# Performance work log

Hardware: AMD Instinct MI355X
Metric: run time of the kernel (lower is better)

## Reference

```python
import jax, jax.numpy as jnp
import numpy as np

B, S, H, DK = 2, 2048, 16, 64
D = H * DK  # d_model = 1024


def setup_inputs() -> dict:
    key = jax.random.key(0)
    ks = jax.random.split(key, 12)
    inp = {
        "queries": jax.random.normal(ks[0], (B, S, D), jnp.float32),
        "keys": jax.random.normal(ks[1], (B, S, D), jnp.float32),
        "values": jax.random.normal(ks[2], (B, S, D), jnp.float32),
        # additive 0/1 mask (1 = masked out), causal upper-triangular
        "mask": jnp.triu(jnp.ones((S, S), jnp.float32), k=1)[None, None, :, :],
        "W_q": jax.random.normal(ks[3], (D, D), jnp.float32) / np.sqrt(D),
        "b_q": jnp.zeros((D,), jnp.float32),
        "W_k": jax.random.normal(ks[4], (D, D), jnp.float32) / np.sqrt(D),
        "b_k": jnp.zeros((D,), jnp.float32),
        "W_v": jax.random.normal(ks[5], (D, D), jnp.float32) / np.sqrt(D),
        "b_v": jnp.zeros((D,), jnp.float32),
        "W_o": jax.random.normal(ks[6], (D, D), jnp.float32) / np.sqrt(D),
        "b_o": jnp.zeros((D,), jnp.float32),
    }
    return inp


def _split_heads(x):
    # (B, S, D) -> (B, H, S, DK)
    return x.reshape(x.shape[0], x.shape[1], H, DK).transpose(0, 2, 1, 3)


def reference(queries, keys, values, mask, W_q, b_q, W_k, b_k, W_v, b_v, W_o, b_o):
    q = _split_heads(queries @ W_q + b_q)  # (B, H, S, DK)
    k = _split_heads(keys @ W_k + b_k)
    v = _split_heads(values @ W_v + b_v)
    scale = 1.0 / jnp.sqrt(jnp.asarray(DK, q.dtype))
    scores = jnp.einsum("bhqd,bhkd->bhqk", q, k) * scale  # (B, H, S, S)
    scores = scores + (-1e9) * mask
    weights = jax.nn.softmax(scores, axis=-1)
    o = jnp.einsum("bhqk,bhkd->bhqd", weights, v)  # (B, H, S, DK)
    o = o.transpose(0, 2, 1, 3).reshape(queries.shape[0], queries.shape[1], D)
    return o @ W_o + b_o
```

## Files before the change

### kernel.cpp

```cpp
#include <hip/hip_runtime.h>
#include <hip/hip_bf16.h>
#include <stdint.h>

typedef unsigned short u16;
typedef __attribute__((ext_vector_type(4))) float f32x4;
typedef __attribute__((ext_vector_type(8))) short bf16x8;

#define B_ 2
#define S_ 2048
#define H_ 16
#define D_ 1024
#define XELEMS (B_*S_*D_)
#define WELEMS (D_*D_)

__device__ __forceinline__ u16 f2bf(float f) {
  union { float f; unsigned u; } v; v.f = f;
  unsigned r = v.u + 0x7fffu + ((v.u >> 16) & 1u);
  return (u16)(r >> 16);
}

__device__ __forceinline__ void async16(const void* g, void* l) {
  __builtin_amdgcn_global_load_lds(
      (const __attribute__((address_space(1))) unsigned int*)g,
      (__attribute__((address_space(3))) unsigned int*)l, 16, 0, 0);
}

#if __has_builtin(__builtin_amdgcn_exp2f)
#define EXP2(x) __builtin_amdgcn_exp2f(x)
#else
#define EXP2(x) exp2f(x)
#endif

__device__ __forceinline__ unsigned cvtpk(float a, float b) {
  unsigned r;
  asm("v_cvt_pk_bf16_f32 %0, %1, %2" : "=v"(r) : "v"(a), "v"(b));
  return r;
}

__global__ __launch_bounds__(256) void prep_k(
    const float* __restrict__ q, const float* __restrict__ k,
    const float* __restrict__ v,
    const float* __restrict__ Wq, const float* __restrict__ Wk,
    const float* __restrict__ Wv, const float* __restrict__ Wo,
    u16* __restrict__ X, u16* __restrict__ WT) {
  const int bid = blockIdx.x;
  if (bid < 4096) {
    __shared__ float tile[32][33];
    const int z = bid >> 10, rem = bid & 1023;
    const float* W = (z == 0) ? Wq : (z == 1) ? Wk : (z == 2) ? Wv : Wo;
    u16* o = WT + z * WELEMS;
    const int r0 = (rem >> 5) << 5, c0 = (rem & 31) << 5;
    const int tx = threadIdx.x & 31, ty = threadIdx.x >> 5;
    #pragma unroll
    for (int rr = ty; rr < 32; rr += 8)
      tile[rr][tx] = W[(r0 + rr) * D_ + c0 + tx];
    __syncthreads();
    #pragma unroll
    for (int rr = ty; rr < 32; rr += 8)
      o[(c0 + rr) * D_ + r0 + tx] = f2bf(tile[tx][rr]);
  } else {
    const int cb = bid - 4096;
    const int ngrp = XELEMS / 8;
    const int total = 3 * ngrp;
    for (int i = cb * 256 + threadIdx.x; i < total; i += 1024 * 256) {
      int which = i / ngrp;
      int off = (i - which * ngrp) * 8;
      const float* src = (which == 0) ? q : (which == 1) ? k : v;
      float4 a = *(const float4*)(src + off);
      float4 b = *(const float4*)(src + off + 4);
      u16 rr[8] = {f2bf(a.x), f2bf(a.y), f2bf(a.z), f2bf(a.w),
                   f2bf(b.x), f2bf(b.y), f2bf(b.z), f2bf(b.w)};
      uint4 pk;
      pk.x = (unsigned)rr[0] | ((unsigned)rr[1] << 16);
      pk.y = (unsigned)rr[2] | ((unsigned)rr[3] << 16);
      pk.z = (unsigned)rr[4] | ((unsigned)rr[5] << 16);
      pk.w = (unsigned)rr[6] | ((unsigned)rr[7] << 16);
      *(uint4*)(X + which * XELEMS + off) = pk;
    }
  }
}

template <int MODE, int DBUF>
__device__ __forceinline__ void gemm_body(const u16* __restrict__ A,
                                          const u16* __restrict__ BT,
                                          const float* __restrict__ bias,
                                          void* __restrict__ outp,
                                          int bm, int bn) {
  constexpr int SMEM_BYTES = DBUF ? 65536 : (MODE == 2 ? 34816 : 32768);
  __shared__ __align__(16) char smem[SMEM_BYTES];
  const int tid = threadIdx.x;
  const int w = tid >> 6, l = tid & 63;
  const int wr = w >> 1, wc = w & 1;
  const int g = l >> 4, r = l & 15;
  (void)w; (void)l;

  f32x4 acc[4][4];
  #pragma unroll
  for (int i = 0; i < 4; i++)
    #pragma unroll
    for (int j = 0; j < 4; j++) acc[i][j] = (f32x4){0.f, 0.f, 0.f, 0.f};

  int dst[4], aoff[4], boff[4];
  #pragma unroll
  for (int i = 0; i < 4; i++) {
    const int o = i * 4096 + tid * 16;
    dst[i] = o;
    const int row = o >> 7;
    const int cbyte = (o & 127) ^ ((row & 7) << 4);
    aoff[i] = (bm + row) * 1024 + (cbyte >> 1);
    boff[i] = (bn + row) * 1024 + (cbyte >> 1);
  }

  if (DBUF == 0) {
    char* Ab = smem;
    char* Bb = smem + 16384;
    for (int t = 0; t < 16; ++t) {
      const int k0 = t * 64;
      #pragma unroll
      for (int i = 0; i < 4; i++) async16(A + aoff[i] + k0, Ab + dst[i]);
      #pragma unroll
      for (int i = 0; i < 4; i++) async16(BT + boff[i] + k0, Bb + dst[i]);
      __syncthreads();
      bf16x8 af[2][4], bf[2][4];
      #pragma unroll
      for (int kk = 0; kk < 2; kk++)
        #pragma unroll
        for (int mi = 0; mi < 4; mi++) {
          const int rA = wr * 64 + mi * 16 + r;
          af[kk][mi] = *(const bf16x8*)(Ab +
              ((rA * 128 + kk * 64 + g * 16) ^ ((rA & 7) << 4)));
        }
      #pragma unroll
      for (int kk = 0; kk < 2; kk++)
        #pragma unroll
        for (int ni = 0; ni < 4; ni++) {
          const int rB = wc * 64 + ni * 16 + r;
          bf[kk][ni] = *(const bf16x8*)(Bb +
              ((rB * 128 + kk * 64 + g * 16) ^ ((rB & 7) << 4)));
        }
      #pragma unroll
      for (int kk = 0; kk < 2; kk++)
        #pragma unroll
        for (int mi = 0; mi < 4; mi++)
          #pragma unroll
          for (int ni = 0; ni < 4; ni++)
            acc[mi][ni] = __builtin_amdgcn_mfma_f32_16x16x32_bf16(
                af[kk][mi], bf[kk][ni], acc[mi][ni], 0, 0, 0);
      __syncthreads();
    }
  } else {
    #pragma unroll
    for (int i = 0; i < 4; i++) {
      async16(A + aoff[i], smem + dst[i]);
      async16(BT + boff[i], smem + 16384 + dst[i]);
    }
    for (int t = 0; t < 16; ++t) {
      const int buf = t & 1;
      const char* Ab = smem + buf * 32768;
      const char* Bb = Ab + 16384;
      if (t < 15) {
        const int k0 = (t + 1) * 64;
        char* An = smem + (buf ^ 1) * 32768;
        #pragma unroll
        for (int i = 0; i < 4; i++) {
          async16(A + aoff[i] + k0, An + dst[i]);
          async16(BT + boff[i] + k0, An + 16384 + dst[i]);
        }
        asm volatile("s_waitcnt vmcnt(8)" ::: "memory");
      } else {
        asm volatile("s_waitcnt vmcnt(0)" ::: "memory");
      }
      asm volatile("s_barrier" ::: "memory");

      bf16x8 af[2][4], bf[2][4];
      #pragma unroll
      for (int kk = 0; kk < 2; kk++)
        #pragma unroll
        for (int mi = 0; mi < 4; mi++) {
          const int rA = wr * 64 + mi * 16 + r;
          af[kk][mi] = *(const bf16x8*)(Ab +
              ((rA * 128 + kk * 64 + g * 16) ^ ((rA & 7) << 4)));
        }
      #pragma unroll
      for (int kk = 0; kk < 2; kk++)
        #pragma unroll
        for (int ni = 0; ni < 4; ni++) {
          const int rB = wc * 64 + ni * 16 + r;
          bf[kk][ni] = *(const bf16x8*)(Bb +
              ((rB * 128 + kk * 64 + g * 16) ^ ((rB & 7) << 4)));
        }
      __builtin_amdgcn_s_setprio(1);
      #pragma unroll
      for (int kk = 0; kk < 2; kk++)
        #pragma unroll
        for (int mi = 0; mi < 4; mi++)
          #pragma unroll
          for (int ni = 0; ni < 4; ni++)
            acc[mi][ni] = __builtin_amdgcn_mfma_f32_16x16x32_bf16(
                af[kk][mi], bf[kk][ni], acc[mi][ni], 0, 0, 0);
      __builtin_amdgcn_s_setprio(0);
      asm volatile("s_barrier" ::: "memory");
    }
  }

  const int col0 = bn + wc * 64;
  float bc[4];
  #pragma unroll
  for (int ni = 0; ni < 4; ni++) bc[ni] = bias[col0 + ni * 16 + r];

  if (MODE == 0) {
    u16* out = (u16*)outp;
    #pragma unroll
    for (int mi = 0; mi < 4; mi++) {
      const int row = bm + wr * 64 + mi * 16 + g * 4;
      #pragma unroll
      for (int ni = 0; ni < 4; ni++) {
        const int col = col0 + ni * 16 + r;
        const int h = col >> 6, dk = col & 63;
        #pragma unroll
        for (int i = 0; i < 4; i++) {
          const int rr = row + i;
          const int b = rr >> 11, s = rr & 2047;
          out[(((b << 4) | h) * 2048 + s) * 64 + dk] =
              f2bf(acc[mi][ni][i] + bc[ni]);
        }
      }
    }
  } else if (MODE == 2) {
    u16* Ts = (u16*)smem;
    #pragma unroll
    for (int mi = 0; mi < 4; mi++) {
      const int lrow = wr * 64 + mi * 16 + g * 4;
      #pragma unroll
      for (int ni = 0; ni < 4; ni++) {
        const int lcol = wc * 64 + ni * 16 + r;
        u16 p0 = f2bf(acc[mi][ni][0] + bc[ni]);
        u16 p1 = f2bf(acc[mi][ni][1] + bc[ni]);
        u16 p2 = f2bf(acc[mi][ni][2] + bc[ni]);
        u16 p3 = f2bf(acc[mi][ni][3] + bc[ni]);
        uint2 pk;
        pk.x = (unsigned)p0 | ((unsigned)p1 << 16);
        pk.y = (unsigned)p2 | ((unsigned)p3 << 16);
        *(uint2*)&Ts[lcol * 136 + lrow] = pk;
      }
    }
    __syncthreads();
    u16* out = (u16*)outp;
    const int bb = bm >> 11;
    const int sbase = bm & 2047;
    #pragma unroll
    for (int j = 0; j < 8; j++) {
      const int c = (tid >> 6) * 512 + j * 64 + (tid & 63);
      const int dk = c >> 4, sc = c & 15;
      const int col = bn + dk;
      const int h = col >> 6, dkk = col & 63;
      bf16x8 vv = *(const bf16x8*)&Ts[dk * 136 + sc * 8];
      *(bf16x8*)&out[(((size_t)(((bb << 4) | h) * 64 + dkk)) << 11) +
                     sbase + sc * 8] = vv;
    }
  } else {
    float* out = (float*)outp;
    #pragma unroll
    for (int mi = 0; mi < 4; mi++) {
      const int row = bm + wr * 64 + mi * 16 + g * 4;
      #pragma unroll
      for (int ni = 0; ni < 4; ni++) {
        const int col = col0 + ni * 16 + r;
        #pragma unroll
        for (int i = 0; i < 4; i++)
          out[(row + i) * 1024 + col] = acc[mi][ni][i] + bc[ni];
      }
    }
  }
}

__global__ __launch_bounds__(256) void gemm_qkv_k(
    const u16* __restrict__ X, const u16* __restrict__ WT,
    const float* __restrict__ bq, const float* __restrict__ bk,
    const float* __restrict__ bv, u16* __restrict__ QKV) {
  const int z = blockIdx.z;
  const float* bias = (z == 0) ? bq : (z == 1) ? bk : bv;
  if (z == 2)
    gemm_body<2, 0>(X + z * XELEMS, WT + z * WELEMS, bias, QKV + z * XELEMS,
                    blockIdx.x * 128, blockIdx.y * 128);
  else
    gemm_body<0, 0>(X + z * XELEMS, WT + z * WELEMS, bias, QKV + z * XELEMS,
                    blockIdx.x * 128, blockIdx.y * 128);
}

__global__ __launch_bounds__(256) void gemm_o_k(
    const u16* __restrict__ O, const u16* __restrict__ WOT,
    const float* __restrict__ bo, float* __restrict__ out) {
  gemm_body<1, 1>(O, WOT, bo, out, blockIdx.x * 128, blockIdx.y * 128);
}

__global__ __launch_bounds__(256) void attn_k(
    const u16* __restrict__ Qh, const u16* __restrict__ Kh,
    const u16* __restrict__ VTh, u16* __restrict__ O) {
  __shared__ __align__(16) char ldsK[2][8192];
  __shared__ __align__(16) char ldsV[2][8192];
  __shared__ __align__(16) u16 ldsP[4][16 * 72];

  const int bh = blockIdx.y;
  const int pj = blockIdx.x;
  const int tid = threadIdx.x;
  const int w = tid >> 6, l = tid & 63;
  const int g = l >> 4, r = l & 15;
  const int b = bh >> 4, h = bh & 15;

  const u16* Qp = Qh + bh * (S_ * 64);
  const char* Kp = (const char*)(Kh + bh * (S_ * 64));
  const char* Vp = (const char*)(VTh + bh * (64 * S_));

  int kdst[2], ksrc[2], vfix[2];
  #pragma unroll
  for (int i = 0; i < 2; i++) {
    const int o = (w * 2 + i) * 1024 + l * 16;
    kdst[i] = o;
    ksrc[i] = o ^ (((o >> 7) & 7) << 4);
    const int d = o >> 7, cbyte = o & 127;
    vfix[i] = d * (S_ * 2) + (cbyte ^ ((d & 7) << 4));
  }
  u16* Pq = &ldsP[w][0];

  #pragma unroll
  for (int pass = 0; pass < 2; pass++) {
    const int qt = pass ? (31 - pj) : pj;
    const int q0w = qt * 64 + w * 16;
    const int nt = qt + 1;
    const int qloc = w * 16 + r;

    bf16x8 qf[2];
    #pragma unroll
    for (int dh = 0; dh < 2; dh++)
      qf[dh] = *(const bf16x8*)(Qp + (q0w + r) * 64 + dh * 32 + g * 8);
    asm volatile("s_waitcnt vmcnt(0)" ::: "memory");

    f32x4 accT[4];
    #pragma unroll
    for (int dn = 0; dn < 4; dn++) accT[dn] = (f32x4){0.f, 0.f, 0.f, 0.f};
    float mrun = -1e30f, lsum = 0.f;

    #pragma unroll
    for (int i = 0; i < 2; i++) {
      async16(Kp + ksrc[i], &ldsK[0][0] + kdst[i]);
      async16(Vp + vfix[i], &ldsV[0][0] + kdst[i]);
    }

    for (int t = 0; t < nt; ++t) {
      const int buf = t & 1;
      if (t + 1 < nt) {
        const char* Ks = Kp + (t + 1) * 8192;
        const char* Vs = Vp + (t + 1) * 128;
        #pragma unroll
        for (int i = 0; i < 2; i++) {
          async16(Ks + ksrc[i], &ldsK[buf ^ 1][0] + kdst[i]);
          async16(Vs + vfix[i], &ldsV[buf ^ 1][0] + kdst[i]);
        }
        asm volatile("s_waitcnt vmcnt(4)" ::: "memory");
      } else {
        asm volatile("s_waitcnt vmcnt(0)" ::: "memory");
      }
      asm volatile("s_barrier" ::: "memory");

      const char* Kb = &ldsK[buf][0];
      f32x4 sc[4];
      #pragma unroll
      for (int ct = 0; ct < 4; ct++) {
        const int row = ct * 16 + r;
        const int sw = (row & 7) << 4;
        bf16x8 k0 = *(const bf16x8*)(Kb + ((row * 128 + g * 16) ^ sw));
        bf16x8 k1 = *(const bf16x8*)(Kb + ((row * 128 + 64 + g * 16) ^ sw));
        f32x4 z = (f32x4){0.f, 0.f, 0.f, 0.f};
        z = __builtin_amdgcn_mfma_f32_16x16x32_bf16(k0, qf[0], z, 0, 0, 0);
        sc[ct] = __builtin_amdgcn_mfma_f32_16x16x32_bf16(k1, qf[1], z, 0, 0, 0);
      }

      const bool diag = (t == nt - 1);
      #pragma unroll
      for (int ct = 0; ct < 4; ct++)
        #pragma unroll
        for (int i = 0; i < 4; i++) {
          float s = sc[ct][i] * 0.18033688f;
          if (diag && (ct * 16 + g * 4 + i > qloc)) s = -1e9f;
          sc[ct][i] = s;
        }

      float a0 = fmaxf(fmaxf(sc[0][0], sc[0][1]), sc[0][2]);
      float a1 = fmaxf(fmaxf(sc[0][3], sc[1][0]), sc[1][1]);
      float a2 = fmaxf(fmaxf(sc[1][2], sc[1][3]), sc[2][0]);
      float a3 = fmaxf(fmaxf(sc[2][1], sc[2][2]), sc[2][3]);
      float a4 = fmaxf(fmaxf(sc[3][0], sc[3][1]), sc[3][2]);
      float pmax = fmaxf(fmaxf(fmaxf(a0, a1), fmaxf(a2, a3)),
                         fmaxf(a4, sc[3][3]));
      pmax = fmaxf(pmax, __shfl_xor(pmax, 16, 64));
      pmax = fmaxf(pmax, __shfl_xor(pmax, 32, 64));

      if (!__all(pmax - mrun <= 11.0f)) {
        const float mnew = fmaxf(mrun, pmax);
        const float corr = EXP2(mrun - mnew);
        mrun = mnew;
        #pragma unroll
        for (int dn = 0; dn < 4; dn++)
          #pragma unroll
          for (int i = 0; i < 4; i++) accT[dn][i] *= corr;
        lsum *= corr;
      }

      float ps = 0.f;
      #pragma unroll
      for (int ct = 0; ct < 4; ct++)
        #pragma unroll
        for (int i = 0; i < 4; i++) {
          const float p = EXP2(sc[ct][i] - mrun);
          sc[ct][i] = p;
          ps += p;
        }
      ps += __shfl_xor(ps, 16, 64);
      ps += __shfl_xor(ps, 32, 64);
      lsum += ps;

      #pragma unroll
      for (int ct = 0; ct < 4; ct++) {
        uint2 pk;
        pk.x = cvtpk(sc[ct][0], sc[ct][1]);
        pk.y = cvtpk(sc[ct][2], sc[ct][3]);
        *(uint2*)&Pq[r * 72 + ct * 16 + g * 4] = pk;
      }
      asm volatile("s_waitcnt lgkmcnt(0)" ::: "memory");

      const char* Vb = &ldsV[buf][0];
      bf16x8 pf[2];
      #pragma unroll
      for (int kp = 0; kp < 2; kp++)
        pf[kp] = *(const bf16x8*)&Pq[r * 72 + kp * 32 + g * 8];
      __builtin_amdgcn_s_setprio(1);
      #pragma unroll
      for (int dn = 0; dn < 4; dn++) {
        const int vrow = dn * 16 + r;
        const int vsw = (vrow & 7) << 4;
        #pragma unroll
        for (int kp = 0; kp < 2; kp++) {
          bf16x8 vf = *(const bf16x8*)(Vb + ((vrow * 128 + kp * 64 + g * 16) ^ vsw));
          accT[dn] = __builtin_amdgcn_mfma_f32_16x16x32_bf16(vf, pf[kp], accT[dn], 0, 0, 0);
        }
      }
      __builtin_amdgcn_s_setprio(0);
      asm volatile("s_barrier" ::: "memory");
    }

    const float inv = 1.0f / lsum;
    const int qrow = q0w + r;
    #pragma unroll
    for (int dn = 0; dn < 4; dn++) {
      u16 o0 = f2bf(accT[dn][0] * inv), o1 = f2bf(accT[dn][1] * inv);
      u16 o2 = f2bf(accT[dn][2] * inv), o3 = f2bf(accT[dn][3] * inv);
      uint2 pk;
      pk.x = (unsigned)o0 | ((unsigned)o1 << 16);
      pk.y = (unsigned)o2 | ((unsigned)o3 << 16);
      *(uint2*)(O + ((size_t)(b * 2048 + qrow)) * 1024 + h * 64 + dn * 16 + g * 4) = pk;
    }
  }
}

extern "C" void kernel_launch(void* const* d_in, const int* in_sizes, int n_in,
                              void* d_out, int out_size, void* d_ws, size_t ws_size,
                              hipStream_t stream) {
  const float* q  = (const float*)d_in[0];
  const float* k  = (const float*)d_in[1];
  const float* v  = (const float*)d_in[2];
  const float* Wq = (const float*)d_in[4];
  const float* bq = (const float*)d_in[5];
  const float* Wk = (const float*)d_in[6];
  const float* bk = (const float*)d_in[7];
  const float* Wv = (const float*)d_in[8];
  const float* bv = (const float*)d_in[9];
  const float* Wo = (const float*)d_in[10];
  const float* bo = (const float*)d_in[11];

  char* ws = (char*)d_ws;
  const size_t MB = 1u << 20;
  u16* X   = (u16*)(ws);
  u16* WT  = (u16*)(ws + 24 * MB);
  u16* QKV = (u16*)(ws + 32 * MB);
  u16* O   = (u16*)(ws);

  hipLaunchKernelGGL(prep_k, dim3(5120), dim3(256), 0, stream,
                     q, k, v, Wq, Wk, Wv, Wo, X, WT);
  hipLaunchKernelGGL(gemm_qkv_k, dim3(32, 8, 3), dim3(256), 0, stream,
                     X, WT, bq, bk, bv, QKV);
  hipLaunchKernelGGL(attn_k, dim3(16, 32), dim3(256), 0, stream,
                     QKV, QKV + XELEMS, QKV + 2 * XELEMS, O);
  hipLaunchKernelGGL(gemm_o_k, dim3(32, 8), dim3(256), 0, stream,
                     O, WT + 3 * WELEMS, bo, (float*)d_out);
}
```

Measured before the change: 128.8 us.

## Run both causal query tiles concurrently in one 512-thread block sharing K/V tiles

The attention kernel now uses 8 waves per block. Two groups of four waves process the paired query tiles (pj and 31-pj) at the same time, sharing each K/V tile loaded into LDS, where before the same block handled the two tiles in two sequential passes. The softmax scale is also folded into the Q projection epilogue, which removes a multiply per score. This halves K/V reloads for the shorter tile and adds parallelism per block. In exchange, the short-tile group sits idle through later iterations while still taking part in the barriers, and the larger block may reduce occupancy.

Result: faster. 124.7 us (-3.2%).

```diff
diff --git a/kernel.cpp b/kernel.cpp
--- a/kernel.cpp
+++ b/kernel.cpp
@@ -12,6 +12,7 @@
 #define D_ 1024
 #define XELEMS (B_*S_*D_)
 #define WELEMS (D_*D_)
+#define QSCALE 0.18033688f
 
 __device__ __forceinline__ u16 f2bf(float f) {
   union { float f; unsigned u; } v; v.f = f;
@@ -85,7 +86,7 @@
                                           const u16* __restrict__ BT,
                                           const float* __restrict__ bias,
                                           void* __restrict__ outp,
-                                          int bm, int bn) {
+                                          int bm, int bn, float scale) {
   constexpr int SMEM_BYTES = DBUF ? 65536 : (MODE == 2 ? 34816 : 32768);
   __shared__ __align__(16) char smem[SMEM_BYTES];
   const int tid = threadIdx.x;
@@ -222,7 +223,7 @@
           const int rr = row + i;
           const int b = rr >> 11, s = rr & 2047;
           out[(((b << 4) | h) * 2048 + s) * 64 + dk] =
-              f2bf(acc[mi][ni][i] + bc[ni]);
+              f2bf((acc[mi][ni][i] + bc[ni]) * scale);
         }
       }
     }
@@ -282,29 +283,31 @@
   const float* bias = (z == 0) ? bq : (z == 1) ? bk : bv;
   if (z == 2)
     gemm_body<2, 0>(X + z * XELEMS, WT + z * WELEMS, bias, QKV + z * XELEMS,
-                    blockIdx.x * 128, blockIdx.y * 128);
+                    blockIdx.x * 128, blockIdx.y * 128, 1.0f);
   else
     gemm_body<0, 0>(X + z * XELEMS, WT + z * WELEMS, bias, QKV + z * XELEMS,
-                    blockIdx.x * 128, blockIdx.y * 128);
+                    blockIdx.x * 128, blockIdx.y * 128,
+                    (z == 0) ? QSCALE : 1.0f);
 }
 
 __global__ __launch_bounds__(256) void gemm_o_k(
     const u16* __restrict__ O, const u16* __restrict__ WOT,
     const float* __restrict__ bo, float* __restrict__ out) {
-  gemm_body<1, 1>(O, WOT, bo, out, blockIdx.x * 128, blockIdx.y * 128);
-}
-
-__global__ __launch_bounds__(256) void attn_k(
+  gemm_body<1, 1>(O, WOT, bo, out, blockIdx.x * 128, blockIdx.y * 128, 1.0f);
+}
+
+__global__ __launch_bounds__(512) void attn_k(
     const u16* __restrict__ Qh, const u16* __restrict__ Kh,
     const u16* __restrict__ VTh, u16* __restrict__ O) {
   __shared__ __align__(16) char ldsK[2][8192];
   __shared__ __align__(16) char ldsV[2][8192];
-  __shared__ __align__(16) u16 ldsP[4][16 * 72];
+  __shared__ __align__(16) u16 ldsP[8][16 * 72];
 
   const int bh = blockIdx.y;
   const int pj = blockIdx.x;
   const int tid = threadIdx.x;
   const int w = tid >> 6, l = tid & 63;
+  const int grp = w >> 2, wg = w & 3;
   const int g = l >> 4, r = l & 15;
   const int b = bh >> 4, h = bh & 15;
 
@@ -312,57 +315,45 @@
   const char* Kp = (const char*)(Kh + bh * (S_ * 64));
   const char* Vp = (const char*)(VTh + bh * (64 * S_));
 
-  int kdst[2], ksrc[2], vfix[2];
-  #pragma unroll
-  for (int i = 0; i < 2; i++) {
-    const int o = (w * 2 + i) * 1024 + l * 16;
-    kdst[i] = o;
-    ksrc[i] = o ^ (((o >> 7) & 7) << 4);
-    const int d = o >> 7, cbyte = o & 127;
-    vfix[i] = d * (S_ * 2) + (cbyte ^ ((d & 7) << 4));
-  }
+  const int o = w * 1024 + l * 16;
+  const int kdst = o;
+  const int ksrc = o ^ (((o >> 7) & 7) << 4);
+  const int vd = o >> 7, vcb = o & 127;
+  const int vfix = vd * (S_ * 2) + (vcb ^ ((vd & 7) << 4));
   u16* Pq = &ldsP[w][0];
 
-  #pragma unroll
-  for (int pass = 0; pass < 2; pass++) {
-    const int qt = pass ? (31 - pj) : pj;
-    const int q0w = qt * 64 + w * 16;
-    const int nt = qt + 1;
-    const int qloc = w * 16 + r;
-
-    bf16x8 qf[2];
-    #pragma unroll
-    for (int dh = 0; dh < 2; dh++)
-      qf[dh] = *(const bf16x8*)(Qp + (q0w + r) * 64 + dh * 32 + g * 8);
-    asm volatile("s_waitcnt vmcnt(0)" ::: "memory");
-
-    f32x4 accT[4];
-    #pragma unroll
-    for (int dn = 0; dn < 4; dn++) accT[dn] = (f32x4){0.f, 0.f, 0.f, 0.f};
-    float mrun = -1e30f, lsum = 0.f;
-
-    #pragma unroll
-    for (int i = 0; i < 2; i++) {
-      async16(Kp + ksrc[i], &ldsK[0][0] + kdst[i]);
-      async16(Vp + vfix[i], &ldsV[0][0] + kdst[i]);
-    }
-
-    for (int t = 0; t < nt; ++t) {
-      const int buf = t & 1;
-      if (t + 1 < nt) {
-        const char* Ks = Kp + (t + 1) * 8192;
-        const char* Vs = Vp + (t + 1) * 128;
-        #pragma unroll
-        for (int i = 0; i < 2; i++) {
-          async16(Ks + ksrc[i], &ldsK[buf ^ 1][0] + kdst[i]);
-          async16(Vs + vfix[i], &ldsV[buf ^ 1][0] + kdst[i]);
-        }
-        asm volatile("s_waitcnt vmcnt(4)" ::: "memory");
-      } else {
-        asm volatile("s_waitcnt vmcnt(0)" ::: "memory");
-      }
-      asm volatile("s_barrier" ::: "memory");
-
+  const int qt = grp ? (31 - pj) : pj;
+  const int q0w = qt * 64 + wg * 16;
+  const int my_nt = qt + 1;
+  const int nt_max = 32 - pj;
+  const int qloc = wg * 16 + r;
+
+  bf16x8 qf[2];
+  #pragma unroll
+  for (int dh = 0; dh < 2; dh++)
+    qf[dh] = *(const bf16x8*)(Qp + (q0w + r) * 64 + dh * 32 + g * 8);
+  asm volatile("s_waitcnt vmcnt(0)" ::: "memory");
+
+  f32x4 accT[4];
+  #pragma unroll
+  for (int dn = 0; dn < 4; dn++) accT[dn] = (f32x4){0.f, 0.f, 0.f, 0.f};
+  float mrun = -1e30f, lsum = 0.f;
+
+  async16(Kp + ksrc, &ldsK[0][0] + kdst);
+  async16(Vp + vfix, &ldsV[0][0] + kdst);
+
+  for (int t = 0; t < nt_max; ++t) {
+    const int buf = t & 1;
+    if (t + 1 < nt_max) {
+      async16(Kp + (t + 1) * 8192 + ksrc, &ldsK[buf ^ 1][0] + kdst);
+      async16(Vp + (t + 1) * 128 + vfix, &ldsV[buf ^ 1][0] + kdst);
+      asm volatile("s_waitcnt vmcnt(2)" ::: "memory");
+    } else {
+      asm volatile("s_waitcnt vmcnt(0)" ::: "memory");
+    }
+    asm volatile("s_barrier" ::: "memory");
+
+    if (t < my_nt) {
       const char* Kb = &ldsK[buf][0];
       f32x4 sc[4];
       #pragma unroll
@@ -376,15 +367,13 @@
         sc[ct] = __builtin_amdgcn_mfma_f32_16x16x32_bf16(k1, qf[1], z, 0, 0, 0);
       }
 
-      const bool diag = (t == nt - 1);
-      #pragma unroll
-      for (int ct = 0; ct < 4; ct++)
-        #pragma unroll
-        for (int i = 0; i < 4; i++) {
-          float s = sc[ct][i] * 0.18033688f;
-          if (diag && (ct * 16 + g * 4 + i > qloc)) s = -1e9f;
-          sc[ct][i] = s;
-        }
+      if (t == my_nt - 1) {
+        #pragma unroll
+        for (int ct = 0; ct < 4; ct++)
+          #pragma unroll
+          for (int i = 0; i < 4; i++)
+            if (ct * 16 + g * 4 + i > qloc) sc[ct][i] = -1e9f;
+      }
 
       float a0 = fmaxf(fmaxf(sc[0][0], sc[0][1]), sc[0][2]);
       float a1 = fmaxf(fmaxf(sc[0][3], sc[1][0]), sc[1][1]);
@@ -446,20 +435,20 @@
         }
       }
       __builtin_amdgcn_s_setprio(0);
-      asm volatile("s_barrier" ::: "memory");
-    }
-
-    const float inv = 1.0f / lsum;
-    const int qrow = q0w + r;
-    #pragma unroll
-    for (int dn = 0; dn < 4; dn++) {
-      u16 o0 = f2bf(accT[dn][0] * inv), o1 = f2bf(accT[dn][1] * inv);
-      u16 o2 = f2bf(accT[dn][2] * inv), o3 = f2bf(accT[dn][3] * inv);
-      uint2 pk;
-      pk.x = (unsigned)o0 | ((unsigned)o1 << 16);
-      pk.y = (unsigned)o2 | ((unsigned)o3 << 16);
-      *(uint2*)(O + ((size_t)(b * 2048 + qrow)) * 1024 + h * 64 + dn * 16 + g * 4) = pk;
-    }
+    }
+    asm volatile("s_barrier" ::: "memory");
+  }
+
+  const float inv = 1.0f / lsum;
+  const int qrow = q0w + r;
+  #pragma unroll
+  for (int dn = 0; dn < 4; dn++) {
+    u16 o0 = f2bf(accT[dn][0] * inv), o1 = f2bf(accT[dn][1] * inv);
+    u16 o2 = f2bf(accT[dn][2] * inv), o3 = f2bf(accT[dn][3] * inv);
+    uint2 pk;
+    pk.x = (unsigned)o0 | ((unsigned)o1 << 16);
+    pk.y = (unsigned)o2 | ((unsigned)o3 << 16);
+    *(uint2*)(O + ((size_t)(b * 2048 + qrow)) * 1024 + h * 64 + dn * 16 + g * 4) = pk;
   }
 }
 
@@ -489,7 +478,7 @@
                      q, k, v, Wq, Wk, Wv, Wo, X, WT);
   hipLaunchKernelGGL(gemm_qkv_k, dim3(32, 8, 3), dim3(256), 0, stream,
                      X, WT, bq, bk, bv, QKV);
-  hipLaunchKernelGGL(attn_k, dim3(16, 32), dim3(256), 0, stream,
+  hipLaunchKernelGGL(attn_k, dim3(16, 32), dim3(512), 0, stream,
                      QKV, QKV + XELEMS, QKV + 2 * XELEMS, O);
   hipLaunchKernelGGL(gemm_o_k, dim3(32, 8), dim3(256), 0, stream,
                      O, WT + 3 * WELEMS, bo, (float*)d_out);
```

## Process both causal tiles concurrently per block, fold Q scale into projection, coalesce QK stores

Applied to the files above, without the earlier changes.

The attention kernel no longer runs two sequential passes. Waves are split into two groups: one handles query tile pj and the other handles tile 31-pj, and each wave now owns 32 query rows instead of 16. K/V tiles loaded into LDS are shared by both groups, so the total K/V load count per block drops, and each K/V fragment read from LDS feeds two MFMAs. The softmax scale is folded into the Q projection epilogue, and Q/K outputs are staged through LDS so they can be written as 16-byte coalesced stores. The cost is more registers per wave and idle waves in the shorter group while the longer group finishes its tiles.

Result: slower. 144.8 us (+12.4%).

```diff
diff --git a/kernel.cpp b/kernel.cpp
--- a/kernel.cpp
+++ b/kernel.cpp
@@ -12,6 +12,7 @@
 #define D_ 1024
 #define XELEMS (B_*S_*D_)
 #define WELEMS (D_*D_)
+#define QSCALE 0.18033688f
 
 __device__ __forceinline__ u16 f2bf(float f) {
   union { float f; unsigned u; } v; v.f = f;
@@ -85,8 +86,8 @@
                                           const u16* __restrict__ BT,
                                           const float* __restrict__ bias,
                                           void* __restrict__ outp,
-                                          int bm, int bn) {
-  constexpr int SMEM_BYTES = DBUF ? 65536 : (MODE == 2 ? 34816 : 32768);
+                                          int bm, int bn, float scale) {
+  constexpr int SMEM_BYTES = DBUF ? 65536 : ((MODE == 0 || MODE == 2) ? 34816 : 32768);
   __shared__ __align__(16) char smem[SMEM_BYTES];
   const int tid = threadIdx.x;
   const int w = tid >> 6, l = tid & 63;
@@ -209,22 +210,31 @@
   for (int ni = 0; ni < 4; ni++) bc[ni] = bias[col0 + ni * 16 + r];
 
   if (MODE == 0) {
+    u16* Ts = (u16*)smem;
+    #pragma unroll
+    for (int mi = 0; mi < 4; mi++) {
+      #pragma unroll
+      for (int ni = 0; ni < 4; ni++) {
+        const int lcol = wc * 64 + ni * 16 + r;
+        #pragma unroll
+        for (int i = 0; i < 4; i++) {
+          const int lrow = wr * 64 + mi * 16 + g * 4 + i;
+          Ts[lrow * 136 + lcol] = f2bf((acc[mi][ni][i] + bc[ni]) * scale);
+        }
+      }
+    }
+    __syncthreads();
     u16* out = (u16*)outp;
-    #pragma unroll
-    for (int mi = 0; mi < 4; mi++) {
-      const int row = bm + wr * 64 + mi * 16 + g * 4;
-      #pragma unroll
-      for (int ni = 0; ni < 4; ni++) {
-        const int col = col0 + ni * 16 + r;
-        const int h = col >> 6, dk = col & 63;
-        #pragma unroll
-        for (int i = 0; i < 4; i++) {
-          const int rr = row + i;
-          const int b = rr >> 11, s = rr & 2047;
-          out[(((b << 4) | h) * 2048 + s) * 64 + dk] =
-              f2bf(acc[mi][ni][i] + bc[ni]);
-        }
-      }
+    const int bb = bm >> 11;
+    const int sbase = bm & 2047;
+    #pragma unroll
+    for (int j = 0; j < 8; j++) {
+      const int c = j * 256 + tid;
+      const int row = c >> 4, oct = c & 15;
+      const int col = bn + oct * 8;
+      const int h = col >> 6, dk = col & 63;
+      bf16x8 vv = *(const bf16x8*)&Ts[row * 136 + oct * 8];
+      *(bf16x8*)&out[(((size_t)((bb << 4) | h) * 2048 + sbase + row) << 6) + dk] = vv;
     }
   } else if (MODE == 2) {
     u16* Ts = (u16*)smem;
@@ -282,16 +292,17 @@
   const float* bias = (z == 0) ? bq : (z == 1) ? bk : bv;
   if (z == 2)
     gemm_body<2, 0>(X + z * XELEMS, WT + z * WELEMS, bias, QKV + z * XELEMS,
-                    blockIdx.x * 128, blockIdx.y * 128);
+                    blockIdx.x * 128, blockIdx.y * 128, 1.0f);
   else
     gemm_body<0, 0>(X + z * XELEMS, WT + z * WELEMS, bias, QKV + z * XELEMS,
-                    blockIdx.x * 128, blockIdx.y * 128);
+                    blockIdx.x * 128, blockIdx.y * 128,
+                    (z == 0) ? QSCALE : 1.0f);
 }
 
 __global__ __launch_bounds__(256) void gemm_o_k(
     const u16* __restrict__ O, const u16* __restrict__ WOT,
     const float* __restrict__ bo, float* __restrict__ out) {
-  gemm_body<1, 1>(O, WOT, bo, out, blockIdx.x * 128, blockIdx.y * 128);
+  gemm_body<1, 1>(O, WOT, bo, out, blockIdx.x * 128, blockIdx.y * 128, 1.0f);
 }
 
 __global__ __launch_bounds__(256) void attn_k(
@@ -299,12 +310,13 @@
     const u16* __restrict__ VTh, u16* __restrict__ O) {
   __shared__ __align__(16) char ldsK[2][8192];
   __shared__ __align__(16) char ldsV[2][8192];
-  __shared__ __align__(16) u16 ldsP[4][16 * 72];
+  __shared__ __align__(16) u16 ldsP[4][32 * 72];
 
   const int bh = blockIdx.y;
   const int pj = blockIdx.x;
   const int tid = threadIdx.x;
   const int w = tid >> 6, l = tid & 63;
+  const int grp = w >> 1, wg = w & 1;
   const int g = l >> 4, r = l & 15;
   const int b = bh >> 4, h = bh & 15;
 
@@ -323,117 +335,130 @@
   }
   u16* Pq = &ldsP[w][0];
 
-  #pragma unroll
-  for (int pass = 0; pass < 2; pass++) {
-    const int qt = pass ? (31 - pj) : pj;
-    const int q0w = qt * 64 + w * 16;
-    const int nt = qt + 1;
-    const int qloc = w * 16 + r;
-
-    bf16x8 qf[2];
+  const int qt = grp ? (31 - pj) : pj;
+  const int q0w = qt * 64 + wg * 32;
+  const int my_nt = qt + 1;
+  const int nt_max = 32 - pj;
+
+  bf16x8 qf[2][2];
+  #pragma unroll
+  for (int qq = 0; qq < 2; qq++)
     #pragma unroll
     for (int dh = 0; dh < 2; dh++)
-      qf[dh] = *(const bf16x8*)(Qp + (q0w + r) * 64 + dh * 32 + g * 8);
-    asm volatile("s_waitcnt vmcnt(0)" ::: "memory");
-
-    f32x4 accT[4];
-    #pragma unroll
-    for (int dn = 0; dn < 4; dn++) accT[dn] = (f32x4){0.f, 0.f, 0.f, 0.f};
-    float mrun = -1e30f, lsum = 0.f;
-
-    #pragma unroll
-    for (int i = 0; i < 2; i++) {
-      async16(Kp + ksrc[i], &ldsK[0][0] + kdst[i]);
-      async16(Vp + vfix[i], &ldsV[0][0] + kdst[i]);
-    }
-
-    for (int t = 0; t < nt; ++t) {
-      const int buf = t & 1;
-      if (t + 1 < nt) {
-        const char* Ks = Kp + (t + 1) * 8192;
-        const char* Vs = Vp + (t + 1) * 128;
-        #pragma unroll
-        for (int i = 0; i < 2; i++) {
-          async16(Ks + ksrc[i], &ldsK[buf ^ 1][0] + kdst[i]);
-          async16(Vs + vfix[i], &ldsV[buf ^ 1][0] + kdst[i]);
-        }
-        asm volatile("s_waitcnt vmcnt(4)" ::: "memory");
-      } else {
-        asm volatile("s_waitcnt vmcnt(0)" ::: "memory");
-      }
-      asm volatile("s_barrier" ::: "memory");
-
+      qf[qq][dh] = *(const bf16x8*)(Qp + (q0w + qq * 16 + r) * 64 + dh * 32 + g * 8);
+  asm volatile("s_waitcnt vmcnt(0)" ::: "memory");
+
+  f32x4 accT[2][4];
+  #pragma unroll
+  for (int qq = 0; qq < 2; qq++)
+    #pragma unroll
+    for (int dn = 0; dn < 4; dn++) accT[qq][dn] = (f32x4){0.f, 0.f, 0.f, 0.f};
+  float mrun[2] = {-1e30f, -1e30f}, lsum[2] = {0.f, 0.f};
+
+  #pragma unroll
+  for (int i = 0; i < 2; i++) {
+    async16(Kp + ksrc[i], &ldsK[0][0] + kdst[i]);
+    async16(Vp + vfix[i], &ldsV[0][0] + kdst[i]);
+  }
+
+  for (int t = 0; t < nt_max; ++t) {
+    const int buf = t & 1;
+    if (t + 1 < nt_max) {
+      const char* Ks = Kp + (t + 1) * 8192;
+      const char* Vs = Vp + (t + 1) * 128;
+      #pragma unroll
+      for (int i = 0; i < 2; i++) {
+        async16(Ks + ksrc[i], &ldsK[buf ^ 1][0] + kdst[i]);
+        async16(Vs + vfix[i], &ldsV[buf ^ 1][0] + kdst[i]);
+      }
+      asm volatile("s_waitcnt vmcnt(4)" ::: "memory");
+    } else {
+      asm volatile("s_waitcnt vmcnt(0)" ::: "memory");
+    }
+    asm volatile("s_barrier" ::: "memory");
+
+    if (t < my_nt) {
       const char* Kb = &ldsK[buf][0];
-      f32x4 sc[4];
+      f32x4 sc[2][4];
       #pragma unroll
       for (int ct = 0; ct < 4; ct++) {
         const int row = ct * 16 + r;
         const int sw = (row & 7) << 4;
         bf16x8 k0 = *(const bf16x8*)(Kb + ((row * 128 + g * 16) ^ sw));
         bf16x8 k1 = *(const bf16x8*)(Kb + ((row * 128 + 64 + g * 16) ^ sw));
-        f32x4 z = (f32x4){0.f, 0.f, 0.f, 0.f};
-        z = __builtin_amdgcn_mfma_f32_16x16x32_bf16(k0, qf[0], z, 0, 0, 0);
-        sc[ct] = __builtin_amdgcn_mfma_f32_16x16x32_bf16(k1, qf[1], z, 0, 0, 0);
-      }
-
-      const bool diag = (t == nt - 1);
-      #pragma unroll
-      for (int ct = 0; ct < 4; ct++)
-        #pragma unroll
-        for (int i = 0; i < 4; i++) {
-          float s = sc[ct][i] * 0.18033688f;
-          if (diag && (ct * 16 + g * 4 + i > qloc)) s = -1e9f;
-          sc[ct][i] = s;
-        }
-
-      float a0 = fmaxf(fmaxf(sc[0][0], sc[0][1]), sc[0][2]);
-      float a1 = fmaxf(fmaxf(sc[0][3], sc[1][0]), sc[1][1]);
-      float a2 = fmaxf(fmaxf(sc[1][2], sc[1][3]), sc[2][0]);
-      float a3 = fmaxf(fmaxf(sc[2][1], sc[2][2]), sc[2][3]);
-      float a4 = fmaxf(fmaxf(sc[3][0], sc[3][1]), sc[3][2]);
-      float pmax = fmaxf(fmaxf(fmaxf(a0, a1), fmaxf(a2, a3)),
-                         fmaxf(a4, sc[3][3]));
-      pmax = fmaxf(pmax, __shfl_xor(pmax, 16, 64));
-      pmax = fmaxf(pmax, __shfl_xor(pmax, 32, 64));
-
-      if (!__all(pmax - mrun <= 11.0f)) {
-        const float mnew = fmaxf(mrun, pmax);
-        const float corr = EXP2(mrun - mnew);
-        mrun = mnew;
-        #pragma unroll
-        for (int dn = 0; dn < 4; dn++)
+        #pragma unroll
+        for (int qq = 0; qq < 2; qq++) {
+          f32x4 z = (f32x4){0.f, 0.f, 0.f, 0.f};
+          z = __builtin_amdgcn_mfma_f32_16x16x32_bf16(k0, qf[qq][0], z, 0, 0, 0);
+          sc[qq][ct] = __builtin_amdgcn_mfma_f32_16x16x32_bf16(k1, qf[qq][1], z, 0, 0, 0);
+        }
+      }
+
+      if (t == my_nt - 1) {
+        #pragma unroll
+        for (int qq = 0; qq < 2; qq++) {
+          const int qloc = wg * 32 + qq * 16 + r;
           #pragma unroll
-          for (int i = 0; i < 4; i++) accT[dn][i] *= corr;
-        lsum *= corr;
-      }
-
-      float ps = 0.f;
-      #pragma unroll
-      for (int ct = 0; ct < 4; ct++)
-        #pragma unroll
-        for (int i = 0; i < 4; i++) {
-          const float p = EXP2(sc[ct][i] - mrun);
-          sc[ct][i] = p;
-          ps += p;
-        }
-      ps += __shfl_xor(ps, 16, 64);
-      ps += __shfl_xor(ps, 32, 64);
-      lsum += ps;
-
-      #pragma unroll
-      for (int ct = 0; ct < 4; ct++) {
-        uint2 pk;
-        pk.x = cvtpk(sc[ct][0], sc[ct][1]);
-        pk.y = cvtpk(sc[ct][2], sc[ct][3]);
-        *(uint2*)&Pq[r * 72 + ct * 16 + g * 4] = pk;
+          for (int ct = 0; ct < 4; ct++)
+            #pragma unroll
+            for (int i = 0; i < 4; i++)
+              if (ct * 16 + g * 4 + i > qloc) sc[qq][ct][i] = -1e9f;
+        }
+      }
+
+      #pragma unroll
+      for (int qq = 0; qq < 2; qq++) {
+        float a0 = fmaxf(fmaxf(sc[qq][0][0], sc[qq][0][1]), sc[qq][0][2]);
+        float a1 = fmaxf(fmaxf(sc[qq][0][3], sc[qq][1][0]), sc[qq][1][1]);
+        float a2 = fmaxf(fmaxf(sc[qq][1][2], sc[qq][1][3]), sc[qq][2][0]);
+        float a3 = fmaxf(fmaxf(sc[qq][2][1], sc[qq][2][2]), sc[qq][2][3]);
+        float a4 = fmaxf(fmaxf(sc[qq][3][0], sc[qq][3][1]), sc[qq][3][2]);
+        float pmax = fmaxf(fmaxf(fmaxf(a0, a1), fmaxf(a2, a3)),
+                           fmaxf(a4, sc[qq][3][3]));
+        pmax = fmaxf(pmax, __shfl_xor(pmax, 16, 64));
+        pmax = fmaxf(pmax, __shfl_xor(pmax, 32, 64));
+
+        if (!__all(pmax - mrun[qq] <= 11.0f)) {
+          const float mnew = fmaxf(mrun[qq], pmax);
+          const float corr = EXP2(mrun[qq] - mnew);
+          mrun[qq] = mnew;
+          #pragma unroll
+          for (int dn = 0; dn < 4; dn++)
+            #pragma unroll
+            for (int i = 0; i < 4; i++) accT[qq][dn][i] *= corr;
+          lsum[qq] *= corr;
+        }
+
+        float ps = 0.f;
+        #pragma unroll
+        for (int ct = 0; ct < 4; ct++)
+          #pragma unroll
+          for (int i = 0; i < 4; i++) {
+            const float p = EXP2(sc[qq][ct][i] - mrun[qq]);
+            sc[qq][ct][i] = p;
+            ps += p;
+          }
+        ps += __shfl_xor(ps, 16, 64);
+        ps += __shfl_xor(ps, 32, 64);
+        lsum[qq] += ps;
+
+        #pragma unroll
+        for (int ct = 0; ct < 4; ct++) {
+          uint2 pk;
+          pk.x = cvtpk(sc[qq][ct][0], sc[qq][ct][1]);
+          pk.y = cvtpk(sc[qq][ct][2], sc[qq][ct][3]);
+          *(uint2*)&Pq[(qq * 16 + r) * 72 + ct * 16 + g * 4] = pk;
+        }
       }
       asm volatile("s_waitcnt lgkmcnt(0)" ::: "memory");
 
       const char* Vb = &ldsV[buf][0];
-      bf16x8 pf[2];
-      #pragma unroll
-      for (int kp = 0; kp < 2; kp++)
-        pf[kp] = *(const bf16x8*)&Pq[r * 72 + kp * 32 + g * 8];
+      bf16x8 pf[2][2];
+      #pragma unroll
+      for (int qq = 0; qq < 2; qq++)
+        #pragma unroll
+        for (int kp = 0; kp < 2; kp++)
+          pf[qq][kp] = *(const bf16x8*)&Pq[(qq * 16 + r) * 72 + kp * 32 + g * 8];
       __builtin_amdgcn_s_setprio(1);
       #pragma unroll
       for (int dn = 0; dn < 4; dn++) {
@@ -442,19 +467,25 @@
         #pragma unroll
         for (int kp = 0; kp < 2; kp++) {
           bf16x8 vf = *(const bf16x8*)(Vb + ((vrow * 128 + kp * 64 + g * 16) ^ vsw));
-          accT[dn] = __builtin_amdgcn_mfma_f32_16x16x32_bf16(vf, pf[kp], accT[dn], 0, 0, 0);
+          #pragma unroll
+          for (int qq = 0; qq < 2; qq++)
+            accT[qq][dn] = __builtin_amdgcn_mfma_f32_16x16x32_bf16(
+                vf, pf[qq][kp], accT[qq][dn], 0, 0, 0);
         }
       }
       __builtin_amdgcn_s_setprio(0);
-      asm volatile("s_barrier" ::: "memory");
-    }
-
-    const float inv = 1.0f / lsum;
-    const int qrow = q0w + r;
+    }
+    asm volatile("s_barrier" ::: "memory");
+  }
+
+  #pragma unroll
+  for (int qq = 0; qq < 2; qq++) {
+    const float inv = 1.0f / lsum[qq];
+    const int qrow = q0w + qq * 16 + r;
     #pragma unroll
     for (int dn = 0; dn < 4; dn++) {
-      u16 o0 = f2bf(accT[dn][0] * inv), o1 = f2bf(accT[dn][1] * inv);
-      u16 o2 = f2bf(accT[dn][2] * inv), o3 = f2bf(accT[dn][3] * inv);
+      u16 o0 = f2bf(accT[qq][dn][0] * inv), o1 = f2bf(accT[qq][dn][1] * inv);
+      u16 o2 = f2bf(accT[qq][dn][2] * inv), o3 = f2bf(accT[qq][dn][3] * inv);
       uint2 pk;
       pk.x = (unsigned)o0 | ((unsigned)o1 << 16);
       pk.y = (unsigned)o2 | ((unsigned)o3 << 16);
```
